# Kernel tuning notes

Hardware: AMD Instinct MI355X
Metric: run time of the kernel (lower is better)

Reference implementation:

```python
import jax, jax.numpy as jnp
import numpy as np

OUT_H, OUT_W = 7, 7
SCALE = 0.25
S = 2  # sample_num per bin axis


def _bilinear(img, y, x):
    """Bilinearly sample img[..., H, W] at float coords (y, x).
    y, x have identical shape G; returns img.shape[:-2] + G.
    Matches RoIAlign CUDA interpolation (zero outside [-1, H]/[-1, W])."""
    H, W = img.shape[-2], img.shape[-1]
    valid = (y > -1.0) & (y < H) & (x > -1.0) & (x < W)
    y = jnp.clip(y, 0.0, H - 1)
    x = jnp.clip(x, 0.0, W - 1)
    y0 = jnp.floor(y).astype(jnp.int32)
    x0 = jnp.floor(x).astype(jnp.int32)
    y1 = jnp.minimum(y0 + 1, H - 1)
    x1 = jnp.minimum(x0 + 1, W - 1)
    ly = y - y0
    lx = x - x0
    hy, hx = 1.0 - ly, 1.0 - lx
    v = (hy * hx * img[..., y0, x0] + hy * lx * img[..., y0, x1]
         + ly * hx * img[..., y1, x0] + ly * lx * img[..., y1, x1])
    return jnp.where(valid, v, 0.0)


def setup_inputs() -> dict:
    key = jax.random.key(0)
    k1, k2, k3, k4, k5 = jax.random.split(key, 5)
    N, C, H, W = 2, 256, 200, 200
    R, MH, MW = 512, 128, 128
    features = jax.random.normal(k1, (N, C, H, W), jnp.float32)
    bidx = jax.random.randint(k2, (R,), 0, N)
    xy1 = jax.random.randint(k3, (R, 2), 0, 672)          # x1, y1 (image coords)
    wh = jax.random.randint(k4, (R, 2), 8, 128)           # box sizes in [8,128)
    xy2 = jnp.minimum(xy1 + wh - 1, 799)                  # x2, y2 inclusive
    rois = jnp.concatenate([bidx[:, None].astype(jnp.float32),
                            xy1.astype(jnp.float32),
                            xy2.astype(jnp.float32)], axis=1)  # [R,5]
    batch_masks = jax.random.uniform(k5, (R, MH, MW), jnp.float32)
    # zero-pad beyond each roi's (h, w), mimicking the list->dense packing
    hv = jnp.arange(MH)[None, :] < (xy2[:, 1] - xy1[:, 1] + 1)[:, None]
    wv = jnp.arange(MW)[None, :] < (xy2[:, 0] - xy1[:, 0] + 1)[:, None]
    batch_masks = batch_masks * (hv[:, :, None] & wv[:, None, :]).astype(jnp.float32)
    return {"features": features, "rois": rois, "batch_masks": batch_masks}


def reference(features, rois, batch_masks):
    """Mask-weighted RoIAlign: per-roi bilinear feature samples are weighted by
    the roi's shape mask (bilinearly sampled in roi-relative image coords),
    then average-pooled over the sub-sample grid of each output bin."""
    C = features.shape[1]

    def one_roi(roi, mask):
        b = roi[0].astype(jnp.int32)
        x1, y1, x2, y2 = roi[1], roi[2], roi[3], roi[4]
        roi_start_w = x1 * SCALE
        roi_start_h = y1 * SCALE
        roi_w = jnp.maximum((x2 - x1 + 1.0) * SCALE, 1.0)
        roi_h = jnp.maximum((y2 - y1 + 1.0) * SCALE, 1.0)
        bin_w = roi_w / OUT_W
        bin_h = roi_h / OUT_H
        # sub-sample offsets: (bin + (i+0.5)/S) for i in [0,S)  -> [OUT*S]
        offs = (jnp.arange(S, dtype=jnp.float32) + 0.5) / S
        ys = roi_start_h + (jnp.arange(OUT_H, dtype=jnp.float32)[:, None] + offs[None, :]).reshape(-1) * bin_h
        xs = roi_start_w + (jnp.arange(OUT_W, dtype=jnp.float32)[:, None] + offs[None, :]).reshape(-1) * bin_w
        yy, xx = jnp.meshgrid(ys, xs, indexing='ij')       # [OUT_H*S, OUT_W*S]
        feat = features[b]                                  # [C, H, W]
        vals = _bilinear(feat, yy, xx)                      # [C, OUT_H*S, OUT_W*S]
        # mask weight at the same sample point, in roi-relative image coords
        my = jnp.clip(yy / SCALE - y1, 0.0, y2 - y1)
        mx = jnp.clip(xx / SCALE - x1, 0.0, x2 - x1)
        wgt = _bilinear(mask, my, mx)                       # [OUT_H*S, OUT_W*S]
        v = (vals * wgt).reshape(C, OUT_H, S, OUT_W, S)
        return v.mean(axis=(2, 4))                          # [C, OUT_H, OUT_W]

    return jax.vmap(one_roi)(rois, batch_masks)             # [R, C, OUT_H, OUT_W]
```

## Files before the change

kernel.cpp:

```cpp
#include <hip/hip_runtime.h>
#include <hip/hip_bf16.h>


constexpr int   OUT_H = 7, OUT_W = 7;
constexpr int   NBIN  = OUT_H * OUT_W;
constexpr float SCALE = 0.25f;
constexpr int   S     = 2;
constexpr int   NSAMP = NBIN * S * S;
constexpr int   CG    = 8;
constexpr int   NPAIR = CG / 2;
constexpr int   RDIM  = 34;
constexpr int   RCOLS = 40;
constexpr int   PSTRIDE = RDIM * RCOLS * 2 + 4;

typedef unsigned short ushort_t;

__device__ __forceinline__ unsigned pack_bf16_pair(float e, float o) {
    __hip_bfloat162 h2 = __float22bfloat162_rn(make_float2(e, o));
    unsigned u;
    __builtin_memcpy(&u, &h2, sizeof(u));
    return u;
}

__global__ __launch_bounds__(256, 6)
void roialign_direct_kernel(const float* __restrict__ features,
                            const float* __restrict__ rois,
                            const float* __restrict__ masks,
                            float*       __restrict__ out,
                            int C, int H, int W, int MH, int MW) {
    __shared__ __align__(16) ushort_t s_reg[NPAIR * PSTRIDE];
    __shared__ ushort4 s_idx[NSAMP];
    __shared__ float4  s_w[NSAMP];

    const int cgp = blockIdx.x;
    const int r   = blockIdx.y;
    const int tid = threadIdx.x;

    const float* roi = rois + (size_t)r * 5;
    const int   b  = (int)roi[0];
    const float x1 = roi[1], y1 = roi[2], x2 = roi[3], y2 = roi[4];

    const float roi_start_w = x1 * SCALE;
    const float roi_start_h = y1 * SCALE;
    const float roi_w = fmaxf((x2 - x1 + 1.0f) * SCALE, 1.0f);
    const float roi_h = fmaxf((y2 - y1 + 1.0f) * SCALE, 1.0f);
    const float bin_w = roi_w * (1.0f / OUT_W);
    const float bin_h = roi_h * (1.0f / OUT_H);

    int y_lo = (int)floorf(roi_start_h); y_lo = max(0, min(y_lo, H - 1));
    int x_lo = (int)floorf(roi_start_w); x_lo = max(0, min(x_lo, W - 1));
    const int y_hi = max(y_lo, min((int)floorf(roi_start_h + roi_h) + 1, H - 1));
    const int x_hi = max(x_lo, min((int)floorf(roi_start_w + roi_w) + 1, W - 1));
    const int rows  = min(y_hi - y_lo + 1, RDIM);
    const int x_lo4 = x_lo & ~3;
    const int cols4 = min((x_hi - x_lo4 + 4) >> 2, RCOLS / 4);

    float yy = 0.f, xx = 0.f, m00 = 0.f, m01 = 0.f, m10 = 0.f, m11 = 0.f;
    float mly = 0.f, mlx = 0.f;
    if (tid < NSAMP) {
        const int bin = tid >> 2;
        const int sub = tid & 3;
        const int ph  = bin / OUT_W, pw = bin % OUT_W;
        const int iy  = sub >> 1,   ix = sub & 1;
        yy = roi_start_h + ((float)ph + ((float)iy + 0.5f) * (1.0f / S)) * bin_h;
        xx = roi_start_w + ((float)pw + ((float)ix + 0.5f) * (1.0f / S)) * bin_w;

        const float* msk = masks + (size_t)r * MH * MW;
        float my = fminf(fmaxf(yy * (1.0f / SCALE) - y1, 0.0f), y2 - y1);
        float mx = fminf(fmaxf(xx * (1.0f / SCALE) - x1, 0.0f), x2 - x1);
        my = fminf(fmaxf(my, 0.0f), (float)(MH - 1));
        mx = fminf(fmaxf(mx, 0.0f), (float)(MW - 1));
        const int my0 = (int)floorf(my), mx0 = (int)floorf(mx);
        const int my1 = min(my0 + 1, MH - 1), mx1 = min(mx0 + 1, MW - 1);
        mly = my - (float)my0; mlx = mx - (float)mx0;
        m00 = msk[my0 * MW + mx0];
        m01 = msk[my0 * MW + mx1];
        m10 = msk[my1 * MW + mx0];
        m11 = msk[my1 * MW + mx1];
    }

    {
        const int g    = tid >> 5;
        const int lane = tid & 31;
        const int pr   = g >> 1;
        const int part = g & 1;
        const size_t HWs = (size_t)H * W;
        const float* srcE = features + ((size_t)b * C + (size_t)(cgp * CG + 2 * pr)) * HWs
                          + (size_t)y_lo * W + x_lo4;
        const float* srcO = srcE + HWs;
        unsigned* dp32base = (unsigned*)(s_reg + pr * PSTRIDE);
        const int items = rows * cols4;
        const float rcp = 1.0f / (float)cols4;
#pragma unroll 2
        for (int it = lane + part * 32; it < items; it += 64) {
            int ry = (int)((float)it * rcp);
            int k  = it - ry * cols4;
            if (k >= cols4) { ry++; k -= cols4; }
            if (k < 0)      { ry--; k += cols4; }
            const float4 vE = *(const float4*)(srcE + ry * W + 4 * k);
            const float4 vO = *(const float4*)(srcO + ry * W + 4 * k);
            const int pix = ry * RCOLS + 4 * k;
            uint2 a, c2;
            a.x  = pack_bf16_pair(vE.x, vO.x);
            a.y  = pack_bf16_pair(vE.y, vO.y);
            c2.x = pack_bf16_pair(vE.z, vO.z);
            c2.y = pack_bf16_pair(vE.w, vO.w);
            *(uint2*)(dp32base + pix)     = a;
            *(uint2*)(dp32base + pix + 2) = c2;
        }
    }

    if (tid < NSAMP) {
        const bool valid = (yy > -1.0f) && (yy < (float)H) && (xx > -1.0f) && (xx < (float)W);
        const float mhy = 1.0f - mly, mhx = 1.0f - mlx;
        const float wgt = mhy * mhx * m00 + mhy * mlx * m01
                        + mly * mhx * m10 + mly * mlx * m11;

        const float yc = fminf(fmaxf(yy, 0.0f), (float)(H - 1));
        const float xc = fminf(fmaxf(xx, 0.0f), (float)(W - 1));
        const int y0  = (int)floorf(yc), x0 = (int)floorf(xc);
        const int y1i = min(y0 + 1, H - 1), x1i = min(x0 + 1, W - 1);
        const float ly = yc - (float)y0, lx = xc - (float)x0;
        const float hy = 1.0f - ly,      hx = 1.0f - lx;

        const int ly0 = min(max(y0  - y_lo,  0), RDIM  - 1);
        const int ly1 = min(max(y1i - y_lo,  0), RDIM  - 1);
        const int lx0 = min(max(x0  - x_lo4, 0), RCOLS - 1);
        const int lx1 = min(max(x1i - x_lo4, 0), RCOLS - 1);

        const float scale_all = (valid ? wgt : 0.0f) * (1.0f / (float)(S * S));
        ushort4 o;
        o.x = (ushort_t)((ly0 * RCOLS + lx0) * 4);
        o.y = (ushort_t)((ly0 * RCOLS + lx1) * 4);
        o.z = (ushort_t)((ly1 * RCOLS + lx0) * 4);
        o.w = (ushort_t)((ly1 * RCOLS + lx1) * 4);
        s_idx[tid] = o;
        float4 w4;
        w4.x = hy * hx * scale_all;
        w4.y = hy * lx * scale_all;
        w4.z = ly * hx * scale_all;
        w4.w = ly * lx * scale_all;
        s_w[tid] = w4;
    }
    __syncthreads();

    float accE = 0.0f, accO = 0.0f;
    const int pr  = tid & 3;
    const int bin = tid >> 2;
    if (tid < NSAMP) {
        const char* base = (const char*)s_reg + pr * (PSTRIDE * 2);
#pragma unroll
        for (int sub = 0; sub < 4; ++sub) {
            const int s = bin * 4 + sub;
            const ushort4 off = s_idx[s];
            const float4  w   = s_w[s];
            const unsigned q0 = *(const unsigned*)(base + off.x);
            const unsigned q1 = *(const unsigned*)(base + off.y);
            const unsigned q2 = *(const unsigned*)(base + off.z);
            const unsigned q3 = *(const unsigned*)(base + off.w);
            accE = fmaf(w.x, __uint_as_float(q0 << 16),          accE);
            accO = fmaf(w.x, __uint_as_float(q0 & 0xffff0000u),  accO);
            accE = fmaf(w.y, __uint_as_float(q1 << 16),          accE);
            accO = fmaf(w.y, __uint_as_float(q1 & 0xffff0000u),  accO);
            accE = fmaf(w.z, __uint_as_float(q2 << 16),          accE);
            accO = fmaf(w.z, __uint_as_float(q2 & 0xffff0000u),  accO);
            accE = fmaf(w.w, __uint_as_float(q3 << 16),          accE);
            accO = fmaf(w.w, __uint_as_float(q3 & 0xffff0000u),  accO);
        }
    }
    __syncthreads();

    float* s_out = (float*)s_reg;
    if (tid < NSAMP) {
        s_out[(2 * pr + 0) * NBIN + bin] = accE;
        s_out[(2 * pr + 1) * NBIN + bin] = accO;
    }
    __syncthreads();

    float* outr = out + ((size_t)r * C + (size_t)cgp * CG) * NBIN;
    for (int i = tid; i < CG * NBIN; i += 256)
        outr[i] = s_out[i];
}

__global__ __launch_bounds__(256)
void mask_roialign_kernel(const float* __restrict__ features,
                          const float* __restrict__ rois,
                          const float* __restrict__ masks,
                          float*       __restrict__ out,
                          int C, int H, int W, int MH, int MW) {
    int blk = blockIdx.x;
    int pw  = blk % OUT_W;
    int ph  = (blk / OUT_W) % OUT_H;
    int r   = blk / (OUT_W * OUT_H);
    int c   = threadIdx.x;
    if (c >= C) return;

    const float* roi = rois + (size_t)r * 5;
    int   b  = (int)roi[0];
    float x1 = roi[1], y1 = roi[2], x2 = roi[3], y2 = roi[4];

    float roi_start_w = x1 * SCALE;
    float roi_start_h = y1 * SCALE;
    float roi_w = fmaxf((x2 - x1 + 1.0f) * SCALE, 1.0f);
    float roi_h = fmaxf((y2 - y1 + 1.0f) * SCALE, 1.0f);
    float bin_w = roi_w / (float)OUT_W;
    float bin_h = roi_h / (float)OUT_H;

    const float* fch = features + ((size_t)b * C + c) * (size_t)(H * W);
    const float* msk = masks + (size_t)r * MH * MW;

    float acc = 0.0f;
#pragma unroll
    for (int iy = 0; iy < S; ++iy) {
        float yy = roi_start_h + ((float)ph + ((float)iy + 0.5f) / (float)S) * bin_h;
#pragma unroll
        for (int ix = 0; ix < S; ++ix) {
            float xx = roi_start_w + ((float)pw + ((float)ix + 0.5f) / (float)S) * bin_w;
            bool valid = (yy > -1.0f) && (yy < (float)H) && (xx > -1.0f) && (xx < (float)W);
            float my = fminf(fmaxf(yy / SCALE - y1, 0.0f), fminf(y2 - y1, (float)(MH - 1)));
            float mx = fminf(fmaxf(xx / SCALE - x1, 0.0f), fminf(x2 - x1, (float)(MW - 1)));
            int my0 = (int)floorf(my), mx0 = (int)floorf(mx);
            int my1 = min(my0 + 1, MH - 1), mx1 = min(mx0 + 1, MW - 1);
            float mly = my - my0, mlx = mx - mx0, mhy = 1.0f - mly, mhx = 1.0f - mlx;
            float wgt = mhy * mhx * msk[my0 * MW + mx0] + mhy * mlx * msk[my0 * MW + mx1]
                      + mly * mhx * msk[my1 * MW + mx0] + mly * mlx * msk[my1 * MW + mx1];
            if (valid) {
                float yc = fminf(fmaxf(yy, 0.0f), (float)(H - 1));
                float xc = fminf(fmaxf(xx, 0.0f), (float)(W - 1));
                int y0 = (int)floorf(yc), x0 = (int)floorf(xc);
                int y1i = min(y0 + 1, H - 1), x1i = min(x0 + 1, W - 1);
                float ly = yc - y0, lx = xc - x0, hy = 1.0f - ly, hx = 1.0f - lx;
                float v = hy * hx * fch[y0  * W + x0 ] + hy * lx * fch[y0  * W + x1i]
                        + ly * hx * fch[y1i * W + x0 ] + ly * lx * fch[y1i * W + x1i];
                acc += wgt * v;
            }
        }
    }
    out[((size_t)r * C + c) * (size_t)NBIN + ph * OUT_W + pw] = acc * (1.0f / (S * S));
}

extern "C" void kernel_launch(void* const* d_in, const int* in_sizes, int n_in,
                              void* d_out, int out_size, void* d_ws, size_t ws_size,
                              hipStream_t stream) {
    const float* features = (const float*)d_in[0];
    const float* rois     = (const float*)d_in[1];
    const float* masks    = (const float*)d_in[2];
    float*       out      = (float*)d_out;

    const int R  = in_sizes[1] / 5;
    const int C  = out_size / (R * NBIN);
    const int H  = 200, W = 200;
    const int MH = 128, MW = 128;

    (void)d_ws; (void)ws_size;

    if ((C % CG == 0) && (W % 4 == 0)) {
        roialign_direct_kernel<<<dim3(C / CG, R), dim3(256), 0, stream>>>(
            features, rois, masks, out, C, H, W, MH, MW);
    } else {
        mask_roialign_kernel<<<dim3(R * NBIN), dim3(256), 0, stream>>>(
            features, rois, masks, out, C, H, W, MH, MW);
    }
}
```

Baseline: 180.7 us.

## Precompute per-ROI sample geometry once and swizzle blocks across XCDs

Moves the per-sample mask-weight and bilinear index/weight computation into a separate precompute kernel that runs once per ROI. Previously each of the 32 channel-group blocks per ROI recomputed it. The gather kernel now loads the precomputed tables from workspace and uses a flattened grid with an XCD-aware block swizzle, so blocks of the same ROI share L2. The cost is an extra kernel launch, workspace traffic, and a fallback to the slow path if the workspace is too small.

```diff
diff --git a/kernel.cpp b/kernel.cpp
--- a/kernel.cpp
+++ b/kernel.cpp
@@ -22,22 +22,30 @@
     return u;
 }
 
-__global__ __launch_bounds__(256, 6)
-void roialign_direct_kernel(const float* __restrict__ features,
-                            const float* __restrict__ rois,
-                            const float* __restrict__ masks,
-                            float*       __restrict__ out,
-                            int C, int H, int W, int MH, int MW) {
-    __shared__ __align__(16) ushort_t s_reg[NPAIR * PSTRIDE];
-    __shared__ ushort4 s_idx[NSAMP];
-    __shared__ float4  s_w[NSAMP];
-
-    const int cgp = blockIdx.x;
-    const int r   = blockIdx.y;
+__device__ __forceinline__ void region_bounds(float roi_start_h, float roi_start_w,
+                                              float roi_h, float roi_w, int H, int W,
+                                              int& y_lo, int& x_lo4, int& rows, int& cols4) {
+    int yl = (int)floorf(roi_start_h); yl = max(0, min(yl, H - 1));
+    int xl = (int)floorf(roi_start_w); xl = max(0, min(xl, W - 1));
+    const int y_hi = max(yl, min((int)floorf(roi_start_h + roi_h) + 1, H - 1));
+    const int x_hi = max(xl, min((int)floorf(roi_start_w + roi_w) + 1, W - 1));
+    y_lo  = yl;
+    rows  = min(y_hi - yl + 1, RDIM);
+    x_lo4 = xl & ~3;
+    cols4 = min((x_hi - x_lo4 + 4) >> 2, RCOLS / 4);
+}
+
+__global__ __launch_bounds__(256)
+void geo_precompute_kernel(const float* __restrict__ rois,
+                           const float* __restrict__ masks,
+                           ushort4* __restrict__ gidx,
+                           float4*  __restrict__ gw,
+                           int H, int W, int MH, int MW) {
+    const int r   = blockIdx.x;
     const int tid = threadIdx.x;
+    if (tid >= NSAMP) return;
 
     const float* roi = rois + (size_t)r * 5;
-    const int   b  = (int)roi[0];
     const float x1 = roi[1], y1 = roi[2], x2 = roi[3], y2 = roi[4];
 
     const float roi_start_w = x1 * SCALE;
@@ -47,36 +55,93 @@
     const float bin_w = roi_w * (1.0f / OUT_W);
     const float bin_h = roi_h * (1.0f / OUT_H);
 
-    int y_lo = (int)floorf(roi_start_h); y_lo = max(0, min(y_lo, H - 1));
-    int x_lo = (int)floorf(roi_start_w); x_lo = max(0, min(x_lo, W - 1));
-    const int y_hi = max(y_lo, min((int)floorf(roi_start_h + roi_h) + 1, H - 1));
-    const int x_hi = max(x_lo, min((int)floorf(roi_start_w + roi_w) + 1, W - 1));
-    const int rows  = min(y_hi - y_lo + 1, RDIM);
-    const int x_lo4 = x_lo & ~3;
-    const int cols4 = min((x_hi - x_lo4 + 4) >> 2, RCOLS / 4);
-
-    float yy = 0.f, xx = 0.f, m00 = 0.f, m01 = 0.f, m10 = 0.f, m11 = 0.f;
-    float mly = 0.f, mlx = 0.f;
+    int y_lo, x_lo4, rows, cols4;
+    region_bounds(roi_start_h, roi_start_w, roi_h, roi_w, H, W, y_lo, x_lo4, rows, cols4);
+
+    const int bin = tid >> 2;
+    const int sub = tid & 3;
+    const int ph  = bin / OUT_W, pw = bin % OUT_W;
+    const int iy  = sub >> 1,   ix = sub & 1;
+
+    const float yy = roi_start_h + ((float)ph + ((float)iy + 0.5f) * (1.0f / S)) * bin_h;
+    const float xx = roi_start_w + ((float)pw + ((float)ix + 0.5f) * (1.0f / S)) * bin_w;
+
+    const bool valid = (yy > -1.0f) && (yy < (float)H) && (xx > -1.0f) && (xx < (float)W);
+
+    const float* msk = masks + (size_t)r * MH * MW;
+    float my = fminf(fmaxf(yy * (1.0f / SCALE) - y1, 0.0f), y2 - y1);
+    float mx = fminf(fmaxf(xx * (1.0f / SCALE) - x1, 0.0f), x2 - x1);
+    my = fminf(fmaxf(my, 0.0f), (float)(MH - 1));
+    mx = fminf(fmaxf(mx, 0.0f), (float)(MW - 1));
+    const int my0 = (int)floorf(my), mx0 = (int)floorf(mx);
+    const int my1 = min(my0 + 1, MH - 1), mx1 = min(mx0 + 1, MW - 1);
+    const float mly = my - (float)my0, mlx = mx - (float)mx0;
+    const float mhy = 1.0f - mly,      mhx = 1.0f - mlx;
+    const float wgt = mhy * mhx * msk[my0 * MW + mx0] + mhy * mlx * msk[my0 * MW + mx1]
+                    + mly * mhx * msk[my1 * MW + mx0] + mly * mlx * msk[my1 * MW + mx1];
+
+    const float yc = fminf(fmaxf(yy, 0.0f), (float)(H - 1));
+    const float xc = fminf(fmaxf(xx, 0.0f), (float)(W - 1));
+    const int y0  = (int)floorf(yc), x0 = (int)floorf(xc);
+    const int y1i = min(y0 + 1, H - 1), x1i = min(x0 + 1, W - 1);
+    const float ly = yc - (float)y0, lx = xc - (float)x0;
+    const float hy = 1.0f - ly,      hx = 1.0f - lx;
+
+    const int ly0 = min(max(y0  - y_lo,  0), RDIM  - 1);
+    const int ly1 = min(max(y1i - y_lo,  0), RDIM  - 1);
+    const int lx0 = min(max(x0  - x_lo4, 0), RCOLS - 1);
+    const int lx1 = min(max(x1i - x_lo4, 0), RCOLS - 1);
+
+    const float scale_all = (valid ? wgt : 0.0f) * (1.0f / (float)(S * S));
+    ushort4 o;
+    o.x = (ushort_t)((ly0 * RCOLS + lx0) * 4);
+    o.y = (ushort_t)((ly0 * RCOLS + lx1) * 4);
+    o.z = (ushort_t)((ly1 * RCOLS + lx0) * 4);
+    o.w = (ushort_t)((ly1 * RCOLS + lx1) * 4);
+    float4 w4;
+    w4.x = hy * hx * scale_all;
+    w4.y = hy * lx * scale_all;
+    w4.z = ly * hx * scale_all;
+    w4.w = ly * lx * scale_all;
+    gidx[(size_t)r * NSAMP + tid] = o;
+    gw  [(size_t)r * NSAMP + tid] = w4;
+}
+
+__global__ __launch_bounds__(256, 6)
+void roialign_gather_kernel(const float* __restrict__ features,
+                            const float* __restrict__ rois,
+                            const ushort4* __restrict__ gidx,
+                            const float4*  __restrict__ gw,
+                            float*       __restrict__ out,
+                            int C, int H, int W, int n_cg, int swz) {
+    __shared__ __align__(16) ushort_t s_reg[NPAIR * PSTRIDE];
+    __shared__ ushort4 s_idx[NSAMP];
+    __shared__ float4  s_w[NSAMP];
+
+    int gid = blockIdx.x;
+    if (swz) {
+        const int per_xcd = (int)gridDim.x >> 3;
+        gid = (gid & 7) * per_xcd + (gid >> 3);
+    }
+    const int r   = gid / n_cg;
+    const int cgp = gid - r * n_cg;
+    const int tid = threadIdx.x;
+
+    const float* roi = rois + (size_t)r * 5;
+    const int   b  = (int)roi[0];
+    const float x1 = roi[1], y1 = roi[2], x2 = roi[3], y2 = roi[4];
+
+    const float roi_start_w = x1 * SCALE;
+    const float roi_start_h = y1 * SCALE;
+    const float roi_w = fmaxf((x2 - x1 + 1.0f) * SCALE, 1.0f);
+    const float roi_h = fmaxf((y2 - y1 + 1.0f) * SCALE, 1.0f);
+
+    int y_lo, x_lo4, rows, cols4;
+    region_bounds(roi_start_h, roi_start_w, roi_h, roi_w, H, W, y_lo, x_lo4, rows, cols4);
+
     if (tid < NSAMP) {
-        const int bin = tid >> 2;
-        const int sub = tid & 3;
-        const int ph  = bin / OUT_W, pw = bin % OUT_W;
-        const int iy  = sub >> 1,   ix = sub & 1;
-        yy = roi_start_h + ((float)ph + ((float)iy + 0.5f) * (1.0f / S)) * bin_h;
-        xx = roi_start_w + ((float)pw + ((float)ix + 0.5f) * (1.0f / S)) * bin_w;
-
-        const float* msk = masks + (size_t)r * MH * MW;
-        float my = fminf(fmaxf(yy * (1.0f / SCALE) - y1, 0.0f), y2 - y1);
-        float mx = fminf(fmaxf(xx * (1.0f / SCALE) - x1, 0.0f), x2 - x1);
-        my = fminf(fmaxf(my, 0.0f), (float)(MH - 1));
-        mx = fminf(fmaxf(mx, 0.0f), (float)(MW - 1));
-        const int my0 = (int)floorf(my), mx0 = (int)floorf(mx);
-        const int my1 = min(my0 + 1, MH - 1), mx1 = min(mx0 + 1, MW - 1);
-        mly = my - (float)my0; mlx = mx - (float)mx0;
-        m00 = msk[my0 * MW + mx0];
-        m01 = msk[my0 * MW + mx1];
-        m10 = msk[my1 * MW + mx0];
-        m11 = msk[my1 * MW + mx1];
+        s_idx[tid] = gidx[(size_t)r * NSAMP + tid];
+        s_w[tid]   = gw  [(size_t)r * NSAMP + tid];
     }
 
     {
@@ -109,39 +174,6 @@
             *(uint2*)(dp32base + pix + 2) = c2;
         }
     }
-
-    if (tid < NSAMP) {
-        const bool valid = (yy > -1.0f) && (yy < (float)H) && (xx > -1.0f) && (xx < (float)W);
-        const float mhy = 1.0f - mly, mhx = 1.0f - mlx;
-        const float wgt = mhy * mhx * m00 + mhy * mlx * m01
-                        + mly * mhx * m10 + mly * mlx * m11;
-
-        const float yc = fminf(fmaxf(yy, 0.0f), (float)(H - 1));
-        const float xc = fminf(fmaxf(xx, 0.0f), (float)(W - 1));
-        const int y0  = (int)floorf(yc), x0 = (int)floorf(xc);
-        const int y1i = min(y0 + 1, H - 1), x1i = min(x0 + 1, W - 1);
-        const float ly = yc - (float)y0, lx = xc - (float)x0;
-        const float hy = 1.0f - ly,      hx = 1.0f - lx;
-
-        const int ly0 = min(max(y0  - y_lo,  0), RDIM  - 1);
-        const int ly1 = min(max(y1i - y_lo,  0), RDIM  - 1);
-        const int lx0 = min(max(x0  - x_lo4, 0), RCOLS - 1);
-        const int lx1 = min(max(x1i - x_lo4, 0), RCOLS - 1);
-
-        const float scale_all = (valid ? wgt : 0.0f) * (1.0f / (float)(S * S));
-        ushort4 o;
-        o.x = (ushort_t)((ly0 * RCOLS + lx0) * 4);
-        o.y = (ushort_t)((ly0 * RCOLS + lx1) * 4);
-        o.z = (ushort_t)((ly1 * RCOLS + lx0) * 4);
-        o.w = (ushort_t)((ly1 * RCOLS + lx1) * 4);
-        s_idx[tid] = o;
-        float4 w4;
-        w4.x = hy * hx * scale_all;
-        w4.y = hy * lx * scale_all;
-        w4.z = ly * hx * scale_all;
-        w4.w = ly * lx * scale_all;
-        s_w[tid] = w4;
-    }
     __syncthreads();
 
     float accE = 0.0f, accO = 0.0f;
@@ -252,11 +284,20 @@
     const int H  = 200, W = 200;
     const int MH = 128, MW = 128;
 
-    (void)d_ws; (void)ws_size;
-
-    if ((C % CG == 0) && (W % 4 == 0)) {
-        roialign_direct_kernel<<<dim3(C / CG, R), dim3(256), 0, stream>>>(
-            features, rois, masks, out, C, H, W, MH, MW);
+    const size_t gidx_bytes = (size_t)R * NSAMP * sizeof(ushort4);
+    const size_t gw_bytes   = (size_t)R * NSAMP * sizeof(float4);
+
+    if ((C % CG == 0) && (W % 4 == 0) && ws_size >= gidx_bytes + gw_bytes) {
+        ushort4* gidx = (ushort4*)d_ws;
+        float4*  gw   = (float4*)((char*)d_ws + gidx_bytes);
+        const int n_cg = C / CG;
+        const int nblk = R * n_cg;
+        const int swz  = (nblk % 8 == 0) ? 1 : 0;
+
+        geo_precompute_kernel<<<dim3(R), dim3(256), 0, stream>>>(
+            rois, masks, gidx, gw, H, W, MH, MW);
+        roialign_gather_kernel<<<dim3(nblk), dim3(256), 0, stream>>>(
+            features, rois, gidx, gw, out, C, H, W, n_cg, swz);
     } else {
         mask_roialign_kernel<<<dim3(R * NBIN), dim3(256), 0, stream>>>(
             features, rois, masks, out, C, H, W, MH, MW);
```

After: 196.1 us. 8.5% more time.
